# Kernel optimization log

Hardware: AMD Instinct MI355X
Metric: run time of the kernel (lower is better)

Reference implementation:

```python
import jax, jax.numpy as jnp
import numpy as np

B = 8192
D = 128
MARGIN = 1.0

def setup_inputs() -> dict:
    key = jax.random.key(0)
    k1, k2, k3, k4 = jax.random.split(key, 4)
    z = jax.random.normal(k1, (B, D), dtype=jnp.float32)
    risk = jax.random.normal(k2, (B,), dtype=jnp.float32)
    time = jax.random.uniform(k3, (B,), dtype=jnp.float32)
    event = jax.random.randint(k4, (B,), 0, 2, dtype=jnp.int32)
    return {"z": z, "risk": risk, "time": time, "event": event}

def reference(z, risk, time, event):
    # pair (i, j) contributes when time[i] < time[j] and event[i] == 1
    mask = (time[:, None] < time[None, :]) & (event[:, None] == 1)  # [B, B]
    mask_f = mask.astype(risk.dtype)
    # relu(margin - (risk[j] - risk[i]))
    hinge = jax.nn.relu(MARGIN - (risk[None, :] - risk[:, None]))   # [B, B]
    total = jnp.sum(hinge * mask_f)
    count = jnp.sum(mask_f)
    return jnp.where(count == 0, jnp.zeros((), risk.dtype), total / count)
```

## Files before the change

### kernel.cpp

```cpp
#include <hip/hip_runtime.h>


#define BDIM 8192
#define MARGIN_F 1.0f

__global__ __launch_bounds__(256) void sgr_pair_kernel(
    const float* __restrict__ risk,
    const float* __restrict__ tim,
    const int*   __restrict__ event,
    double*      __restrict__ ws)
{
    __shared__ float s_time[256];
    __shared__ float s_risk[256];

    const int t     = threadIdx.x;
    const int i     = blockIdx.x * 256 + t;
    const int jbase = blockIdx.y * 256;

    s_time[t] = tim[jbase + t];
    s_risk[t] = risk[jbase + t];
    __syncthreads();

    const float ti   = tim[i];
    const float rip1 = risk[i] + MARGIN_F;
    const bool  ev   = (event[i] == 1);

    float sum = 0.0f;
    float cnt = 0.0f;
    if (ev) {
        #pragma unroll 8
        for (int j = 0; j < 256; ++j) {
            const float tj = s_time[j];
            const float rj = s_risk[j];
            const bool  m  = ti < tj;
            const float h  = fmaxf(rip1 - rj, 0.0f);
            sum += m ? h : 0.0f;
            cnt += m ? 1.0f : 0.0f;
        }
    }

    #pragma unroll
    for (int off = 32; off > 0; off >>= 1) {
        sum += __shfl_down(sum, off, 64);
        cnt += __shfl_down(cnt, off, 64);
    }

    __shared__ float w_sum[4];
    __shared__ float w_cnt[4];
    const int wave = t >> 6;
    const int lane = t & 63;
    if (lane == 0) { w_sum[wave] = sum; w_cnt[wave] = cnt; }
    __syncthreads();

    if (t == 0) {
        const float bs = w_sum[0] + w_sum[1] + w_sum[2] + w_sum[3];
        const float bc = w_cnt[0] + w_cnt[1] + w_cnt[2] + w_cnt[3];
        atomicAdd(&ws[0], (double)bs);
        atomicAdd(&ws[1], (double)bc);
    }
}

__global__ void sgr_finalize_kernel(const double* __restrict__ ws,
                                    float* __restrict__ out)
{
    const double cnt = ws[1];
    out[0] = (cnt == 0.0) ? 0.0f : (float)(ws[0] / cnt);
}

extern "C" void kernel_launch(void* const* d_in, const int* in_sizes, int n_in,
                              void* d_out, int out_size, void* d_ws, size_t ws_size,
                              hipStream_t stream)
{
    const float* risk  = (const float*)d_in[1];
    const float* tim   = (const float*)d_in[2];
    const int*   event = (const int*)d_in[3];
    float*       out   = (float*)d_out;
    double*      ws    = (double*)d_ws;

    hipMemsetAsync(ws, 0, 2 * sizeof(double), stream);

    dim3 grid(BDIM / 256, BDIM / 256);
    sgr_pair_kernel<<<grid, 256, 0, stream>>>(risk, tim, event, ws);
    sgr_finalize_kernel<<<1, 1, 0, stream>>>(ws, out);
}
```

Before: 91.77 us.

## Register-block four rows per thread, vector LDS reads, fuse finalize via ticket

Each thread now handles four i rows, so each float4 shared-memory load of time and risk is reused across four rows. Non-event rows get an infinite time so the branch disappears, and the count uses integers. The separate finalize launch is replaced by a last-block ticket that computes the output inside the main kernel. In exchange the grid has 4x fewer blocks, occupancy drops, and register pressure rises.

Result: faster. 84.88 us, median of 2 (-7.5%).

```diff
diff --git a/kernel.cpp b/kernel.cpp
--- a/kernel.cpp
+++ b/kernel.cpp
@@ -1,70 +1,97 @@
 #include <hip/hip_runtime.h>
 
 
-#define BDIM 8192
 #define MARGIN_F 1.0f
+#define B_N   8192
+#define TPB   256
+#define IPT   4
+#define JT    256
+#define GRID_X (B_N / (TPB * IPT))
+#define GRID_Y (B_N / JT)
+#define NBLOCKS (GRID_X * GRID_Y)
 
-__global__ __launch_bounds__(256) void sgr_pair_kernel(
+struct Ws {
+    double total;
+    unsigned int cnt;
+    unsigned int ticket;
+};
+
+__global__ __launch_bounds__(TPB) void sgr_kernel(
     const float* __restrict__ risk,
     const float* __restrict__ tim,
     const int*   __restrict__ event,
-    double*      __restrict__ ws)
+    Ws*          __restrict__ ws,
+    float*       __restrict__ out)
 {
-    __shared__ float s_time[256];
-    __shared__ float s_risk[256];
+    __shared__ float4 s_t4[JT / 4];
+    __shared__ float4 s_r4[JT / 4];
 
     const int t     = threadIdx.x;
-    const int i     = blockIdx.x * 256 + t;
-    const int jbase = blockIdx.y * 256;
+    const int jbase = blockIdx.y * JT;
 
-    s_time[t] = tim[jbase + t];
-    s_risk[t] = risk[jbase + t];
+    ((float*)s_t4)[t] = tim[jbase + t];
+    ((float*)s_r4)[t] = risk[jbase + t];
     __syncthreads();
 
-    const float ti   = tim[i];
-    const float rip1 = risk[i] + MARGIN_F;
-    const bool  ev   = (event[i] == 1);
+    const int ibase = blockIdx.x * (TPB * IPT);
+    float ti[IPT], rip1[IPT], sum[IPT];
+    unsigned int cnt[IPT];
+    #pragma unroll
+    for (int k = 0; k < IPT; ++k) {
+        const int i  = ibase + k * TPB + t;
+        const bool ev = (event[i] == 1);
+        ti[k]   = ev ? tim[i] : __builtin_inff();
+        rip1[k] = risk[i] + MARGIN_F;
+        sum[k]  = 0.0f;
+        cnt[k]  = 0u;
+    }
 
-    float sum = 0.0f;
-    float cnt = 0.0f;
-    if (ev) {
-        #pragma unroll 8
-        for (int j = 0; j < 256; ++j) {
-            const float tj = s_time[j];
-            const float rj = s_risk[j];
-            const bool  m  = ti < tj;
-            const float h  = fmaxf(rip1 - rj, 0.0f);
-            sum += m ? h : 0.0f;
-            cnt += m ? 1.0f : 0.0f;
+    #pragma unroll 4
+    for (int c = 0; c < JT / 4; ++c) {
+        const float4 t4 = s_t4[c];
+        const float4 r4 = s_r4[c];
+        const float tj[4] = {t4.x, t4.y, t4.z, t4.w};
+        const float rj[4] = {r4.x, r4.y, r4.z, r4.w};
+        #pragma unroll
+        for (int u = 0; u < 4; ++u) {
+            #pragma unroll
+            for (int k = 0; k < IPT; ++k) {
+                const bool  m = ti[k] < tj[u];
+                const float h = fmaxf(rip1[k] - rj[u], 0.0f);
+                sum[k] += m ? h : 0.0f;
+                cnt[k] += m ? 1u : 0u;
+            }
         }
     }
 
+    float        s  = (sum[0] + sum[1]) + (sum[2] + sum[3]);
+    unsigned int cu = (cnt[0] + cnt[1]) + (cnt[2] + cnt[3]);
+
     #pragma unroll
     for (int off = 32; off > 0; off >>= 1) {
-        sum += __shfl_down(sum, off, 64);
-        cnt += __shfl_down(cnt, off, 64);
+        s  += __shfl_down(s, off, 64);
+        cu += __shfl_down(cu, off, 64);
     }
 
-    __shared__ float w_sum[4];
-    __shared__ float w_cnt[4];
-    const int wave = t >> 6;
-    const int lane = t & 63;
-    if (lane == 0) { w_sum[wave] = sum; w_cnt[wave] = cnt; }
+    __shared__ float        w_s[TPB / 64];
+    __shared__ unsigned int w_c[TPB / 64];
+    const int wave = t >> 6, lane = t & 63;
+    if (lane == 0) { w_s[wave] = s; w_c[wave] = cu; }
     __syncthreads();
 
     if (t == 0) {
-        const float bs = w_sum[0] + w_sum[1] + w_sum[2] + w_sum[3];
-        const float bc = w_cnt[0] + w_cnt[1] + w_cnt[2] + w_cnt[3];
-        atomicAdd(&ws[0], (double)bs);
-        atomicAdd(&ws[1], (double)bc);
+        const float        bs = (w_s[0] + w_s[1]) + (w_s[2] + w_s[3]);
+        const unsigned int bc = (w_c[0] + w_c[1]) + (w_c[2] + w_c[3]);
+        atomicAdd(&ws->total, (double)bs);
+        atomicAdd(&ws->cnt, bc);
+        __threadfence();
+        const unsigned int old = atomicAdd(&ws->ticket, 1u);
+        if (old == NBLOCKS - 1) {
+            const double       tot = atomicAdd(&ws->total, 0.0);
+            const unsigned int cc  = atomicAdd(&ws->cnt, 0u);
+            out[0] = cc ? (float)(tot / (double)cc) : 0.0f;
+        }
     }
-}
-
-__global__ void sgr_finalize_kernel(const double* __restrict__ ws,
-                                    float* __restrict__ out)
-{
-    const double cnt = ws[1];
-    out[0] = (cnt == 0.0) ? 0.0f : (float)(ws[0] / cnt);
 }
 
 extern "C" void kernel_launch(void* const* d_in, const int* in_sizes, int n_in,
@@ -75,11 +102,10 @@
     const float* tim   = (const float*)d_in[2];
     const int*   event = (const int*)d_in[3];
     float*       out   = (float*)d_out;
-    double*      ws    = (double*)d_ws;
+    Ws*          ws    = (Ws*)d_ws;
 
-    hipMemsetAsync(ws, 0, 2 * sizeof(double), stream);
+    hipMemsetAsync(ws, 0, sizeof(Ws), stream);
 
-    dim3 grid(BDIM / 256, BDIM / 256);
-    sgr_pair_kernel<<<grid, 256, 0, stream>>>(risk, tim, event, ws);
-    sgr_finalize_kernel<<<1, 1, 0, stream>>>(ws, out);
+    dim3 grid(GRID_X, GRID_Y);
+    sgr_kernel<<<grid, TPB, 0, stream>>>(risk, tim, event, ws, out);
 }
```
